# Optimization experiments

Hardware: AMD Instinct MI355X
Metric: run time of the kernel (lower is better)

Reference implementation:

```python
import jax, jax.numpy as jnp
import numpy as np

NEG_BIG = -9.0e15


def masked_mean_softmax(idx):
    # softmax over a 0/-inf mask == uniform weights over positions where idx > 0
    logits = jnp.where(idx > 0, 1.0, NEG_BIG).astype(jnp.float32)
    return jax.nn.softmax(logits, axis=1)


def setup_inputs() -> dict:
    key = jax.random.key(0)
    ks = jax.random.split(key, 8)
    N_NODES, N_EDGES, EDGE_ARITY, NODE_DEG = 100000, 50000, 32, 16
    D_IN, D_OUT, TV = 128, 128, 128
    stdv = 1.0 / np.sqrt(D_IN)
    u = lambda k, shp: jax.random.uniform(k, shp, jnp.float32, -stdv, stdv)
    return {
        "x": jax.random.normal(ks[0], (N_NODES, D_IN), jnp.float32),
        "seq": jax.random.randint(ks[1], (N_EDGES, EDGE_ARITY), 0, N_NODES),
        "useq": jax.random.randint(ks[2], (N_NODES, NODE_DEG), 0, N_EDGES),
        "TextVector": jax.random.normal(ks[3], (TV,), jnp.float32),
        "weight1": u(ks[4], (D_IN, D_OUT)),
        "weight2": u(ks[5], (D_OUT, D_OUT)),
        "weight3": u(ks[6], (TV, TV)),
    }


def reference(x, seq, useq, TextVector, weight1, weight2, weight3):
    # NOTE: the torch module overwrites TextVector with weight3[0]; dropout is
    # a no-op in eval mode and is omitted here.
    tv = weight3[0]                                   # [TV]
    dot = weight3 @ tv                                # [TV]
    cos = dot / (jnp.linalg.norm(tv) * jnp.linalg.norm(weight3, axis=1))
    inter_nw = jnp.mean(cos)                          # scalar

    xw = (x @ weight1) * inter_nw                     # [N, D_OUT]

    nor = masked_mean_softmax(seq)                    # [E, A]
    adj_with_fea = xw[seq]                            # [E, A, D_OUT] gather
    edge = jnp.einsum('eac,ea->ec', adj_with_fea, nor)
    edge = jax.nn.relu(edge)
    e1 = edge @ weight2                               # [E, D_OUT]

    u_nor = masked_mean_softmax(useq)                 # [N, K]
    edge_adj = e1[useq]                               # [N, K, D_OUT] gather
    node = jnp.einsum('nkc,nk->nc', edge_adj, u_nor)  # [N, D_OUT]
    return node
```

## Files before the change

### kernel.cpp

```cpp
#include <hip/hip_runtime.h>
#include <hip/hip_fp16.h>

#define ND 100000
#define NE 50000
#define AR 32
#define DG 16
#define D  128

typedef _Float16 half8_t __attribute__((ext_vector_type(8)));
typedef _Float16 half4_t __attribute__((ext_vector_type(4)));
typedef float    f32x4_t __attribute__((ext_vector_type(4)));

#define APAD 136

__global__ __launch_bounds__(256) void k_prep(const float* __restrict__ w1,
                                              const float* __restrict__ w2,
                                              const float* __restrict__ w3,
                                              _Float16* __restrict__ w1f,
                                              _Float16* __restrict__ w2f,
                                              float* __restrict__ inter_out) {
    if (blockIdx.x == 64) {
        __shared__ float red[128];
        int j = threadIdx.x;
        if (j < 128) {
            float dot = 0.f, sq = 0.f, sq0 = 0.f;
            #pragma unroll 8
            for (int k = 0; k < D; ++k) {
                float wj = w3[j * D + k];
                float w0 = w3[k];
                dot += wj * w0;
                sq  += wj * wj;
                sq0 += w0 * w0;
            }
            red[j] = dot / (sqrtf(sq0) * sqrtf(sq));
        }
        __syncthreads();
        if (j == 0) {
            float s = 0.f;
            for (int i = 0; i < 128; ++i) s += red[i];
            inter_out[0] = s / 128.f;
        }
        return;
    }
    int o = blockIdx.x * 256 + threadIdx.x;
    int j    = o & 7;
    int lane = (o >> 3) & 63;
    int frag = o >> 9;
    int ntile = frag >> 2, ktile = frag & 3;
    int n = ntile * 16 + (lane & 15);
    int k = ktile * 32 + (lane >> 4) * 8 + j;
    w1f[o] = (_Float16)w1[k * D + n];
    w2f[o] = (_Float16)w2[k * D + n];
}

__global__ __launch_bounds__(256) void k_xw(const float* __restrict__ x,
                                            const _Float16* __restrict__ w1f_g,
                                            const float* __restrict__ inter_p,
                                            _Float16* __restrict__ xwh) {
    __shared__ _Float16 wfrag[D * D];
    __shared__ _Float16 xs[64 * APAD];
    int t = threadIdx.x;
    {
        const float4* src = (const float4*)w1f_g;
        float4* dst = (float4*)wfrag;
        #pragma unroll
        for (int i = 0; i < 8; ++i) dst[i * 256 + t] = src[i * 256 + t];
    }
    int rowbase = blockIdx.x * 64;
    #pragma unroll
    for (int p = 0; p < 8; ++p) {
        int idx = p * 1024 + t * 4;
        int r = idx >> 7, c = idx & 127;
        int grow = rowbase + r;
        float4 v = make_float4(0.f, 0.f, 0.f, 0.f);
        if (grow < ND) v = ((const float4*)x)[(size_t)grow * 32 + (c >> 2)];
        half4_t h = { (_Float16)v.x, (_Float16)v.y, (_Float16)v.z, (_Float16)v.w };
        *(half4_t*)&xs[r * APAD + c] = h;
    }
    __syncthreads();

    int wave = t >> 6, lane = t & 63;
    int quad = lane >> 4, l15 = lane & 15;
    int m0 = wave * 16;
    float inter = inter_p[0];

    half8_t a[4];
    #pragma unroll
    for (int kt = 0; kt < 4; ++kt)
        a[kt] = *(const half8_t*)&xs[(m0 + l15) * APAD + kt * 32 + quad * 8];

    #pragma unroll
    for (int nt = 0; nt < 8; ++nt) {
        f32x4_t acc = {0.f, 0.f, 0.f, 0.f};
        #pragma unroll
        for (int kt = 0; kt < 4; ++kt) {
            half8_t b = *(const half8_t*)&wfrag[((nt * 4 + kt) * 64 + lane) * 8];
            acc = __builtin_amdgcn_mfma_f32_16x16x32_f16(a[kt], b, acc, 0, 0, 0);
        }
        int col = nt * 16 + l15;
        #pragma unroll
        for (int i = 0; i < 4; ++i) {
            int grow = rowbase + m0 + quad * 4 + i;
            if (grow < ND)
                xwh[(size_t)grow * D + col] = (_Float16)(acc[i] * inter);
        }
    }
}

__global__ __launch_bounds__(256) void k_gather_e(const int* __restrict__ seq,
                                                  const _Float16* __restrict__ xwh,
                                                  _Float16* __restrict__ ea) {
    __shared__ int srt[16 * AR];
    int t = threadIdx.x;
    int wave = t >> 6, lane = t & 63;
    int e = lane >> 4, l16 = lane & 15;
    int le = wave * 4 + e;
    int eg = blockIdx.x * 16 + le;

    int2 sv = ((const int2*)seq)[(size_t)eg * 16 + l16];
    int sh = e * 16;
    unsigned long long b0 = __ballot(sv.x > 0);
    unsigned long long b1 = __ballot(sv.y > 0);
    unsigned int f0 = (unsigned int)(b0 >> sh) & 0xFFFFu;
    unsigned int f1 = (unsigned int)(b1 >> sh) & 0xFFFFu;
    int cnt = __popc(f0) + __popc(f1);
    bool allv = (cnt == 0);
    if (allv) cnt = AR;
    float wvf = 1.f / (float)cnt;
    bool v0 = (sv.x > 0) | allv, v1 = (sv.y > 0) | allv;
    int key0 = v0 ? (sv.x / 6250) : 16;
    int key1 = v1 ? (sv.y / 6250) : 16;

    unsigned int lowj  = (1u << l16) - 1u;
    unsigned int lowj1 = lowj | (1u << l16);
    int off = 0, r0 = 0, r1 = 0;
    #pragma unroll
    for (int cv = 0; cv <= 16; ++cv) {
        unsigned long long m0 = __ballot(key0 == cv);
        unsigned long long m1 = __ballot(key1 == cv);
        unsigned int g0 = (unsigned int)(m0 >> sh) & 0xFFFFu;
        unsigned int g1 = (unsigned int)(m1 >> sh) & 0xFFFFu;
        if (key0 == cv) r0 = off + __popc(g0 & lowj)  + __popc(g1 & lowj);
        if (key1 == cv) r1 = off + __popc(g0 & lowj1) + __popc(g1 & lowj);
        off += __popc(g0) + __popc(g1);
    }
    srt[le * AR + r0] = sv.x;
    srt[le * AR + r1] = sv.y;

    float acc[8] = {0.f, 0.f, 0.f, 0.f, 0.f, 0.f, 0.f, 0.f};
    int colOff = l16 * 8;
    #pragma unroll
    for (int tg = 0; tg < 8; ++tg) {
        int4 sr = *(const int4*)&srt[le * AR + tg * 4];
        int rows[4] = { sr.x, sr.y, sr.z, sr.w };
        #pragma unroll
        for (int u = 0; u < 4; ++u) {
            int tt = tg * 4 + u;
            float w = (tt < cnt) ? wvf : 0.f;
            half8_t v = *(const half8_t*)(xwh + (size_t)rows[u] * D + colOff);
            #pragma unroll
            for (int jj = 0; jj < 8; ++jj)
                acc[jj] = fmaf(w, (float)v[jj], acc[jj]);
        }
    }
    half8_t h;
    #pragma unroll
    for (int jj = 0; jj < 8; ++jj) h[jj] = (_Float16)fmaxf(acc[jj], 0.f);
    f32x4_t hv = *(f32x4_t*)&h;
    __builtin_nontemporal_store(hv, (f32x4_t*)(ea + (size_t)eg * D + colOff));
}

__global__ __launch_bounds__(256) void k_gemm_e(const _Float16* __restrict__ ea,
                                                const _Float16* __restrict__ w2f_g,
                                                _Float16* __restrict__ e1h) {
    __shared__ _Float16 wfrag[D * D];
    __shared__ _Float16 et[64 * APAD];
    int t = threadIdx.x;
    {
        const float4* src = (const float4*)w2f_g;
        float4* dst = (float4*)wfrag;
        #pragma unroll
        for (int i = 0; i < 8; ++i) dst[i * 256 + t] = src[i * 256 + t];
    }
    int rowbase = blockIdx.x * 64;
    #pragma unroll
    for (int p = 0; p < 4; ++p) {
        int hidx = p * 2048 + t * 8;
        int r = hidx >> 7, c = hidx & 127;
        int grow = rowbase + r;
        int gs = (grow < NE) ? grow : (NE - 1);
        half8_t v = *(const half8_t*)(ea + (size_t)gs * D + c);
        *(half8_t*)&et[r * APAD + c] = v;
    }
    __syncthreads();

    int wave = t >> 6, lane = t & 63;
    int quad = lane >> 4, l15 = lane & 15;
    int m0 = wave * 16;

    half8_t a[4];
    #pragma unroll
    for (int kt = 0; kt < 4; ++kt)
        a[kt] = *(const half8_t*)&et[(m0 + l15) * APAD + kt * 32 + quad * 8];

    #pragma unroll
    for (int nt = 0; nt < 8; ++nt) {
        f32x4_t acc = {0.f, 0.f, 0.f, 0.f};
        #pragma unroll
        for (int kt = 0; kt < 4; ++kt) {
            half8_t b = *(const half8_t*)&wfrag[((nt * 4 + kt) * 64 + lane) * 8];
            acc = __builtin_amdgcn_mfma_f32_16x16x32_f16(a[kt], b, acc, 0, 0, 0);
        }
        int col = nt * 16 + l15;
        #pragma unroll
        for (int i = 0; i < 4; ++i) {
            int grow = rowbase + m0 + quad * 4 + i;
            if (grow < NE)
                e1h[(size_t)grow * D + col] = (_Float16)acc[i];
        }
    }
}

__global__ __launch_bounds__(256) void k_gather_n(const int* __restrict__ useq,
                                                  const _Float16* __restrict__ e1h,
                                                  float* __restrict__ out) {
    __shared__ int srt[16 * DG];
    int t = threadIdx.x;
    int wave = t >> 6, lane = t & 63;
    int nd = lane >> 4, l16 = lane & 15;
    int ln = wave * 4 + nd;
    int ng = blockIdx.x * 16 + ln;

    int sval = useq[(size_t)ng * DG + l16];
    int sh = nd * 16;
    unsigned long long b = __ballot(sval > 0);
    unsigned int f = (unsigned int)(b >> sh) & 0xFFFFu;
    int cnt = __popc(f);
    bool allv = (cnt == 0);
    if (allv) cnt = DG;
    float wvf = 1.f / (float)cnt;
    bool v = (sval > 0) | allv;
    int key = v ? (sval / 3125) : 16;

    unsigned int lowj = (1u << l16) - 1u;
    int off = 0, r = 0;
    #pragma unroll
    for (int cv = 0; cv <= 16; ++cv) {
        unsigned long long m = __ballot(key == cv);
        unsigned int g = (unsigned int)(m >> sh) & 0xFFFFu;
        if (key == cv) r = off + __popc(g & lowj);
        off += __popc(g);
    }
    srt[ln * DG + r] = sval;

    float acc[8] = {0.f, 0.f, 0.f, 0.f, 0.f, 0.f, 0.f, 0.f};
    int colOff = l16 * 8;
    #pragma unroll
    for (int tg = 0; tg < 4; ++tg) {
        int4 sr = *(const int4*)&srt[ln * DG + tg * 4];
        int rows[4] = { sr.x, sr.y, sr.z, sr.w };
        #pragma unroll
        for (int u = 0; u < 4; ++u) {
            int tt = tg * 4 + u;
            float w = (tt < cnt) ? wvf : 0.f;
            half8_t vv = *(const half8_t*)(e1h + (size_t)rows[u] * D + colOff);
            #pragma unroll
            for (int jj = 0; jj < 8; ++jj)
                acc[jj] = fmaf(w, (float)vv[jj], acc[jj]);
        }
    }
    f32x4_t o0 = { acc[0], acc[1], acc[2], acc[3] };
    f32x4_t o1 = { acc[4], acc[5], acc[6], acc[7] };
    f32x4_t* p = (f32x4_t*)(out + (size_t)ng * D + colOff);
    __builtin_nontemporal_store(o0, p);
    __builtin_nontemporal_store(o1, p + 1);
}

extern "C" void kernel_launch(void* const* d_in, const int* in_sizes, int n_in,
                              void* d_out, int out_size, void* d_ws, size_t ws_size,
                              hipStream_t stream) {
    const float* x    = (const float*)d_in[0];
    const int*   seq  = (const int*)d_in[1];
    const int*   useq = (const int*)d_in[2];
    const float* w1   = (const float*)d_in[4];
    const float* w2   = (const float*)d_in[5];
    const float* w3   = (const float*)d_in[6];
    float* out = (float*)d_out;

    _Float16* xwh   = (_Float16*)d_out;
    _Float16* ea    = (_Float16*)d_out + (size_t)ND * D;
    float*    inter = (float*)d_ws;
    _Float16* w1f   = (_Float16*)((char*)d_ws + 256);
    _Float16* w2f   = (_Float16*)((char*)d_ws + 256 + 32768);
    _Float16* e1h   = (_Float16*)((char*)d_ws + 256 + 65536);

    hipLaunchKernelGGL(k_prep,     dim3(65),             dim3(256), 0, stream, w1, w2, w3, w1f, w2f, inter);
    hipLaunchKernelGGL(k_xw,       dim3((ND + 63) / 64), dim3(256), 0, stream, x, w1f, inter, xwh);
    hipLaunchKernelGGL(k_gather_e, dim3(NE / 16),        dim3(256), 0, stream, seq, xwh, ea);
    hipLaunchKernelGGL(k_gemm_e,   dim3((NE + 63) / 64), dim3(256), 0, stream, ea, w2f, e1h);
    hipLaunchKernelGGL(k_gather_n, dim3(ND / 16),        dim3(256), 0, stream, useq, e1h, out);
}
```

Measured before the change: 230.3 us.

## Drop index bucket-sort in gathers, batch loads via shuffles, vectorize GEMM stores

The two gather kernels no longer bucket-sort indices into shared memory by node range. Each lane now broadcasts the row indices with wave shuffles and issues all 16 row loads before accumulating, which exposes more memory-level parallelism and removes the ballot loops. The GEMM kernels swap the MFMA operand order so each lane holds four contiguous output columns of one row, allowing one half4 store instead of four scalar half stores. This gives up the L2 locality the sort provided, and the ea store becomes a normal store instead of a nontemporal one.

```diff
diff --git a/kernel.cpp b/kernel.cpp
--- a/kernel.cpp
+++ b/kernel.cpp
@@ -89,85 +89,70 @@
     for (int kt = 0; kt < 4; ++kt)
         a[kt] = *(const half8_t*)&xs[(m0 + l15) * APAD + kt * 32 + quad * 8];
 
+    int grow = rowbase + m0 + l15;
     #pragma unroll
     for (int nt = 0; nt < 8; ++nt) {
         f32x4_t acc = {0.f, 0.f, 0.f, 0.f};
         #pragma unroll
         for (int kt = 0; kt < 4; ++kt) {
             half8_t b = *(const half8_t*)&wfrag[((nt * 4 + kt) * 64 + lane) * 8];
-            acc = __builtin_amdgcn_mfma_f32_16x16x32_f16(a[kt], b, acc, 0, 0, 0);
-        }
-        int col = nt * 16 + l15;
-        #pragma unroll
-        for (int i = 0; i < 4; ++i) {
-            int grow = rowbase + m0 + quad * 4 + i;
-            if (grow < ND)
-                xwh[(size_t)grow * D + col] = (_Float16)(acc[i] * inter);
-        }
+            acc = __builtin_amdgcn_mfma_f32_16x16x32_f16(b, a[kt], acc, 0, 0, 0);
+        }
+        half4_t hv = { (_Float16)(acc[0] * inter), (_Float16)(acc[1] * inter),
+                       (_Float16)(acc[2] * inter), (_Float16)(acc[3] * inter) };
+        if (grow < ND)
+            *(half4_t*)(xwh + (size_t)grow * D + nt * 16 + quad * 4) = hv;
     }
 }
 
 __global__ __launch_bounds__(256) void k_gather_e(const int* __restrict__ seq,
                                                   const _Float16* __restrict__ xwh,
                                                   _Float16* __restrict__ ea) {
-    __shared__ int srt[16 * AR];
     int t = threadIdx.x;
     int wave = t >> 6, lane = t & 63;
     int e = lane >> 4, l16 = lane & 15;
     int le = wave * 4 + e;
     int eg = blockIdx.x * 16 + le;
-
-    int2 sv = ((const int2*)seq)[(size_t)eg * 16 + l16];
-    int sh = e * 16;
-    unsigned long long b0 = __ballot(sv.x > 0);
-    unsigned long long b1 = __ballot(sv.y > 0);
-    unsigned int f0 = (unsigned int)(b0 >> sh) & 0xFFFFu;
-    unsigned int f1 = (unsigned int)(b1 >> sh) & 0xFFFFu;
+    int base = e * 16;
+
+    int sv0 = seq[(size_t)eg * AR + l16];
+    int sv1 = seq[(size_t)eg * AR + 16 + l16];
+    unsigned long long b0 = __ballot(sv0 > 0);
+    unsigned long long b1 = __ballot(sv1 > 0);
+    unsigned int f0 = (unsigned int)(b0 >> base) & 0xFFFFu;
+    unsigned int f1 = (unsigned int)(b1 >> base) & 0xFFFFu;
     int cnt = __popc(f0) + __popc(f1);
     bool allv = (cnt == 0);
     if (allv) cnt = AR;
-    float wvf = 1.f / (float)cnt;
-    bool v0 = (sv.x > 0) | allv, v1 = (sv.y > 0) | allv;
-    int key0 = v0 ? (sv.x / 6250) : 16;
-    int key1 = v1 ? (sv.y / 6250) : 16;
-
-    unsigned int lowj  = (1u << l16) - 1u;
-    unsigned int lowj1 = lowj | (1u << l16);
-    int off = 0, r0 = 0, r1 = 0;
-    #pragma unroll
-    for (int cv = 0; cv <= 16; ++cv) {
-        unsigned long long m0 = __ballot(key0 == cv);
-        unsigned long long m1 = __ballot(key1 == cv);
-        unsigned int g0 = (unsigned int)(m0 >> sh) & 0xFFFFu;
-        unsigned int g1 = (unsigned int)(m1 >> sh) & 0xFFFFu;
-        if (key0 == cv) r0 = off + __popc(g0 & lowj)  + __popc(g1 & lowj);
-        if (key1 == cv) r1 = off + __popc(g0 & lowj1) + __popc(g1 & lowj);
-        off += __popc(g0) + __popc(g1);
-    }
-    srt[le * AR + r0] = sv.x;
-    srt[le * AR + r1] = sv.y;
-
-    float acc[8] = {0.f, 0.f, 0.f, 0.f, 0.f, 0.f, 0.f, 0.f};
+    float wv = 1.f / (float)cnt;
+
+    float acc[8] = {};
     int colOff = l16 * 8;
     #pragma unroll
-    for (int tg = 0; tg < 8; ++tg) {
-        int4 sr = *(const int4*)&srt[le * AR + tg * 4];
-        int rows[4] = { sr.x, sr.y, sr.z, sr.w };
-        #pragma unroll
-        for (int u = 0; u < 4; ++u) {
-            int tt = tg * 4 + u;
-            float w = (tt < cnt) ? wvf : 0.f;
-            half8_t v = *(const half8_t*)(xwh + (size_t)rows[u] * D + colOff);
+    for (int h = 0; h < 2; ++h) {
+        int sreg = h ? sv1 : sv0;
+        float w[16];
+        const _Float16* addr[16];
+        #pragma unroll
+        for (int u = 0; u < 16; ++u) {
+            int rr = __shfl(sreg, base + u, 64);
+            w[u] = ((rr > 0) | allv) ? wv : 0.f;
+            addr[u] = xwh + (size_t)rr * D + colOff;
+        }
+        half8_t v[16];
+        #pragma unroll
+        for (int u = 0; u < 16; ++u) v[u] = *(const half8_t*)addr[u];
+        #pragma unroll
+        for (int u = 0; u < 16; ++u) {
             #pragma unroll
             for (int jj = 0; jj < 8; ++jj)
-                acc[jj] = fmaf(w, (float)v[jj], acc[jj]);
-        }
-    }
-    half8_t h;
-    #pragma unroll
-    for (int jj = 0; jj < 8; ++jj) h[jj] = (_Float16)fmaxf(acc[jj], 0.f);
-    f32x4_t hv = *(f32x4_t*)&h;
-    __builtin_nontemporal_store(hv, (f32x4_t*)(ea + (size_t)eg * D + colOff));
+                acc[jj] = fmaf(w[u], (float)v[u][jj], acc[jj]);
+        }
+    }
+    half8_t hv;
+    #pragma unroll
+    for (int jj = 0; jj < 8; ++jj) hv[jj] = (_Float16)fmaxf(acc[jj], 0.f);
+    *(half8_t*)(ea + (size_t)eg * D + colOff) = hv;
 }
 
 __global__ __launch_bounds__(256) void k_gemm_e(const _Float16* __restrict__ ea,
@@ -203,71 +188,59 @@
     for (int kt = 0; kt < 4; ++kt)
         a[kt] = *(const half8_t*)&et[(m0 + l15) * APAD + kt * 32 + quad * 8];
 
+    int grow = rowbase + m0 + l15;
     #pragma unroll
     for (int nt = 0; nt < 8; ++nt) {
         f32x4_t acc = {0.f, 0.f, 0.f, 0.f};
         #pragma unroll
         for (int kt = 0; kt < 4; ++kt) {
             half8_t b = *(const half8_t*)&wfrag[((nt * 4 + kt) * 64 + lane) * 8];
-            acc = __builtin_amdgcn_mfma_f32_16x16x32_f16(a[kt], b, acc, 0, 0, 0);
-        }
-        int col = nt * 16 + l15;
-        #pragma unroll
-        for (int i = 0; i < 4; ++i) {
-            int grow = rowbase + m0 + quad * 4 + i;
-            if (grow < NE)
-                e1h[(size_t)grow * D + col] = (_Float16)acc[i];
-        }
+            acc = __builtin_amdgcn_mfma_f32_16x16x32_f16(b, a[kt], acc, 0, 0, 0);
+        }
+        half4_t hv = { (_Float16)acc[0], (_Float16)acc[1],
+                       (_Float16)acc[2], (_Float16)acc[3] };
+        if (grow < NE)
+            *(half4_t*)(e1h + (size_t)grow * D + nt * 16 + quad * 4) = hv;
     }
 }
 
 __global__ __launch_bounds__(256) void k_gather_n(const int* __restrict__ useq,
                                                   const _Float16* __restrict__ e1h,
                                                   float* __restrict__ out) {
-    __shared__ int srt[16 * DG];
     int t = threadIdx.x;
     int wave = t >> 6, lane = t & 63;
     int nd = lane >> 4, l16 = lane & 15;
     int ln = wave * 4 + nd;
     int ng = blockIdx.x * 16 + ln;
+    int base = nd * 16;
 
     int sval = useq[(size_t)ng * DG + l16];
-    int sh = nd * 16;
     unsigned long long b = __ballot(sval > 0);
-    unsigned int f = (unsigned int)(b >> sh) & 0xFFFFu;
+    unsigned int f = (unsigned int)(b >> base) & 0xFFFFu;
     int cnt = __popc(f);
     bool allv = (cnt == 0);
     if (allv) cnt = DG;
-    float wvf = 1.f / (float)cnt;
-    bool v = (sval > 0) | allv;
-    int key = v ? (sval / 3125) : 16;
-
-    unsigned int lowj = (1u << l16) - 1u;
-    int off = 0, r = 0;
-    #pragma unroll
-    for (int cv = 0; cv <= 16; ++cv) {
-        unsigned long long m = __ballot(key == cv);
-        unsigned int g = (unsigned int)(m >> sh) & 0xFFFFu;
-        if (key == cv) r = off + __popc(g & lowj);
-        off += __popc(g);
-    }
-    srt[ln * DG + r] = sval;
-
-    float acc[8] = {0.f, 0.f, 0.f, 0.f, 0.f, 0.f, 0.f, 0.f};
+    float wv = 1.f / (float)cnt;
+
     int colOff = l16 * 8;
-    #pragma unroll
-    for (int tg = 0; tg < 4; ++tg) {
-        int4 sr = *(const int4*)&srt[ln * DG + tg * 4];
-        int rows[4] = { sr.x, sr.y, sr.z, sr.w };
-        #pragma unroll
-        for (int u = 0; u < 4; ++u) {
-            int tt = tg * 4 + u;
-            float w = (tt < cnt) ? wvf : 0.f;
-            half8_t vv = *(const half8_t*)(e1h + (size_t)rows[u] * D + colOff);
-            #pragma unroll
-            for (int jj = 0; jj < 8; ++jj)
-                acc[jj] = fmaf(w, (float)vv[jj], acc[jj]);
-        }
+    float w[16];
+    const _Float16* addr[16];
+    #pragma unroll
+    for (int u = 0; u < 16; ++u) {
+        int rr = __shfl(sval, base + u, 64);
+        w[u] = ((rr > 0) | allv) ? wv : 0.f;
+        addr[u] = e1h + (size_t)rr * D + colOff;
+    }
+    half8_t v[16];
+    #pragma unroll
+    for (int u = 0; u < 16; ++u) v[u] = *(const half8_t*)addr[u];
+
+    float acc[8] = {};
+    #pragma unroll
+    for (int u = 0; u < 16; ++u) {
+        #pragma unroll
+        for (int jj = 0; jj < 8; ++jj)
+            acc[jj] = fmaf(w[u], (float)v[u][jj], acc[jj]);
     }
     f32x4_t o0 = { acc[0], acc[1], acc[2], acc[3] };
     f32x4_t o1 = { acc[4], acc[5], acc[6], acc[7] };
```

Result: no change. 232.1 us (+0.8%).
